# Performance work log

Measured on AMD Instinct MI355X. Metric: run time of the kernel, lower is better.

The kernel has to match this reference:

```python
import math
import jax, jax.numpy as jnp
import numpy as np

B, T, D = 512, 512, 256
ALPHA = 0.5
BETA = 0.9


def setup_inputs() -> dict:
    key = jax.random.key(0)
    ks = jax.random.split(key, 9)
    s = 1.0 / math.sqrt(D)
    return {
        "window_features": jax.random.normal(ks[0], (B, T, D), jnp.float32),
        "timestamps": jax.random.uniform(ks[1], (B, T), jnp.float32) * 86400.0 * 7,
        "prev_L": jax.random.normal(ks[2], (B, D), jnp.float32),
        "prev_M": jax.random.uniform(ks[3], (B, 1), jnp.float32),
        "pad_mask": jnp.zeros((B, T), jnp.bool_),
        "W_Q": jax.random.normal(ks[4], (D, D), jnp.float32) * s,
        "W_K": jax.random.normal(ks[5], (D, D), jnp.float32) * s,
        "W_V": jax.random.normal(ks[6], (D, D), jnp.float32) * s,
        "cls_w": jax.random.normal(ks[7], (1, 2 * D + 1), jnp.float32) * s,
        "cls_b": jnp.zeros((1,), jnp.float32),
    }


def reference(window_features, timestamps, prev_L, prev_M, pad_mask,
              W_Q, W_K, W_V, cls_w, cls_b):
    Bv, Tv, d = window_features.shape
    valid = ~pad_mask
    valid_f = valid.astype(window_features.dtype)              # [B,T]
    valid_count = jnp.clip(valid_f.sum(1, keepdims=True), 1.0)  # [B,1]

    # decay weights from recency (days)
    t_masked = jnp.where(pad_mask, -1e18, timestamps)
    t_max = t_masked.max(1, keepdims=True)                      # [B,1]
    dt = jnp.clip(t_max - timestamps, 0.0) / 86400.0
    lam = jnp.exp(-ALPHA * dt) * valid_f                        # [B,T]

    # mean-pooled query
    q = (window_features * valid_f[..., None]).sum(1) / valid_count  # [B,d]
    Q = q @ W_Q.T                                               # [B,d]
    K = jnp.einsum('btd,ed->bte', window_features, W_K)         # [B,T,d]
    V = jnp.einsum('btd,ed->bte', window_features, W_V)         # [B,T,d]

    scores = jnp.einsum('bd,btd->bt', Q, K) / math.sqrt(d)      # [B,T]
    scores = jnp.where(pad_mask, -1e9, scores)
    attn = jax.nn.softmax(scores, axis=-1)

    # decay-modulated reweighting + renormalization
    w = lam * attn
    w = w / (w.sum(1, keepdims=True) + 1e-8)

    L_t = jnp.einsum('bt,btd->bd', w, V)                        # [B,d]
    delta_t = L_t - prev_L
    M_t = BETA * prev_M + (1.0 - BETA) * jnp.linalg.norm(delta_t, axis=1, keepdims=True)
    T_event = jnp.concatenate([L_t, delta_t, M_t], axis=-1)     # [B,2d+1]
    p = (T_event @ cls_w.T + cls_b).squeeze(-1)                 # [B]
    return (p, T_event, L_t, M_t)
```

## Files before the change

kernel.cpp:

```cpp
#include <hip/hip_runtime.h>
#include <math.h>

#define ALPHA 0.5f
#define BETA 0.9f
#define Bsz 512
#define Tsz 512
#define Dsz 256
#define TILE 32
#define NTILE (Tsz / TILE)

__device__ __forceinline__ float wave_reduce_sum(float v) {
    v += __shfl_xor(v, 32, 64);
    v += __shfl_xor(v, 16, 64);
    v += __shfl_xor(v, 8, 64);
    v += __shfl_xor(v, 4, 64);
    v += __shfl_xor(v, 2, 64);
    v += __shfl_xor(v, 1, 64);
    return v;
}

__device__ __forceinline__ float wave_reduce_max(float v) {
    v = fmaxf(v, __shfl_xor(v, 32, 64));
    v = fmaxf(v, __shfl_xor(v, 16, 64));
    v = fmaxf(v, __shfl_xor(v, 8, 64));
    v = fmaxf(v, __shfl_xor(v, 4, 64));
    v = fmaxf(v, __shfl_xor(v, 2, 64));
    v = fmaxf(v, __shfl_xor(v, 1, 64));
    return v;
}

__device__ __forceinline__ void load_lds16(const float* g, float* l) {
    __builtin_amdgcn_global_load_lds(
        (const __attribute__((address_space(1))) void*)(g),
        (__attribute__((address_space(3))) void*)(l),
        16, 0, 0);
}

__global__ __launch_bounds__(256) void fused(const float* __restrict__ x,
                                             const float* __restrict__ ts,
                                             const unsigned char* __restrict__ pad,
                                             const float* __restrict__ WQ,
                                             const float* __restrict__ WK,
                                             const float* __restrict__ WV,
                                             const float* __restrict__ prevL,
                                             const float* __restrict__ prevM,
                                             const float* __restrict__ clsw,
                                             const float* __restrict__ clsb,
                                             float* __restrict__ out) {
    const int b = blockIdx.x;
    const int tid = threadIdx.x;
    const int w = tid >> 6, lane = tid & 63;
    const int rloc = lane >> 3;
    const int sub = lane & 7;

    __shared__ __align__(16) float buf[2][TILE][Dsz];
    __shared__ float lamS[Tsz];
    __shared__ float okS[Tsz];
    __shared__ float part[4][Dsz];
    __shared__ float qS[Dsz];
    __shared__ float QS[Dsz];
    __shared__ __align__(16) float qkS[Dsz];
    __shared__ float gS[TILE];
    __shared__ float xwS[Dsz];
    __shared__ float EGS[8];
    __shared__ float red[8];
    __shared__ float red2[4];
    __shared__ float tmaxS, cntS;

    float lmax = -1e30f;
    float lcnt = 0.f;
    for (int t = tid; t < Tsz; t += 256) {
        bool v = (pad[(size_t)b * Tsz + t] == 0);
        float tv = ts[(size_t)b * Tsz + t];
        okS[t] = v ? 1.f : 0.f;
        lamS[t] = tv;
        if (v) { lmax = fmaxf(lmax, tv); lcnt += 1.f; }
    }
    lmax = wave_reduce_max(lmax);
    lcnt = wave_reduce_sum(lcnt);
    if (lane == 0) { red[w] = lmax; red[4 + w] = lcnt; }
    __syncthreads();
    if (tid == 0) {
        tmaxS = fmaxf(fmaxf(red[0], red[1]), fmaxf(red[2], red[3]));
        cntS = fmaxf(red[4] + red[5] + red[6] + red[7], 1.f);
    }
    __syncthreads();

    const float tmax = tmaxS;
    for (int t = tid; t < Tsz; t += 256) {
        float dt = fmaxf(tmax - lamS[t], 0.f) * (1.f / 86400.f);
        lamS[t] = okS[t] * __expf(-ALPHA * dt);
    }

    const float* xb = x + (size_t)b * Tsz * Dsz;
    float4 a0 = make_float4(0.f, 0.f, 0.f, 0.f);
    float4 a1 = a0, a2 = a0, a3 = a0;
    const int tbase = w * 128;
    for (int i = 0; i < 128; i += 4) {
        const int t = tbase + i;
        float4 x0 = *(const float4*)(xb + (size_t)(t + 0) * Dsz + lane * 4);
        float4 x1 = *(const float4*)(xb + (size_t)(t + 1) * Dsz + lane * 4);
        float4 x2 = *(const float4*)(xb + (size_t)(t + 2) * Dsz + lane * 4);
        float4 x3 = *(const float4*)(xb + (size_t)(t + 3) * Dsz + lane * 4);
        const float v0 = okS[t], v1 = okS[t + 1], v2 = okS[t + 2], v3 = okS[t + 3];
        a0.x += v0 * x0.x; a0.y += v0 * x0.y; a0.z += v0 * x0.z; a0.w += v0 * x0.w;
        a1.x += v1 * x1.x; a1.y += v1 * x1.y; a1.z += v1 * x1.z; a1.w += v1 * x1.w;
        a2.x += v2 * x2.x; a2.y += v2 * x2.y; a2.z += v2 * x2.z; a2.w += v2 * x2.w;
        a3.x += v3 * x3.x; a3.y += v3 * x3.y; a3.z += v3 * x3.z; a3.w += v3 * x3.w;
    }
    float4 accq;
    accq.x = (a0.x + a1.x) + (a2.x + a3.x);
    accq.y = (a0.y + a1.y) + (a2.y + a3.y);
    accq.z = (a0.z + a1.z) + (a2.z + a3.z);
    accq.w = (a0.w + a1.w) + (a2.w + a3.w);
    part[w][lane * 4 + 0] = accq.x;
    part[w][lane * 4 + 1] = accq.y;
    part[w][lane * 4 + 2] = accq.z;
    part[w][lane * 4 + 3] = accq.w;

    {
        const int t0 = (NTILE - 1) * TILE;
        #pragma unroll
        for (int k = 0; k < 8; ++k) {
            const int r = w * 8 + k;
            load_lds16(xb + (size_t)(t0 + r) * Dsz + lane * 4, &buf[0][r][0]);
        }
    }
    __syncthreads();

    qS[tid] = (part[0][tid] + part[1][tid] + part[2][tid] + part[3][tid]) / cntS;
    __syncthreads();

    float Qi = 0.f;
    const float* wqrow = WQ + (size_t)tid * Dsz;
    #pragma unroll 4
    for (int d4 = 0; d4 < Dsz; d4 += 4) {
        float4 wv = *(const float4*)(wqrow + d4);
        Qi += wv.x * qS[d4] + wv.y * qS[d4 + 1] + wv.z * qS[d4 + 2] + wv.w * qS[d4 + 3];
    }
    QS[tid] = Qi;
    __syncthreads();

    {
        float v0 = 0.f, v1 = 0.f, v2 = 0.f, v3 = 0.f;
        #pragma unroll 4
        for (int e = 0; e < Dsz; e += 4) {
            v0 += QS[e + 0] * WK[(size_t)(e + 0) * Dsz + tid];
            v1 += QS[e + 1] * WK[(size_t)(e + 1) * Dsz + tid];
            v2 += QS[e + 2] * WK[(size_t)(e + 2) * Dsz + tid];
            v3 += QS[e + 3] * WK[(size_t)(e + 3) * Dsz + tid];
        }
        qkS[tid] = ((v0 + v1) + (v2 + v3)) * 0.0625f;
    }
    __syncthreads();

    float4 qkr[8];
    #pragma unroll
    for (int jj = 0; jj < 8; ++jj)
        qkr[jj] = *(const float4*)(&qkS[(jj * 8 + sub) << 2]);

    float4 acc = make_float4(0.f, 0.f, 0.f, 0.f);
    float E = 0.f, G = 0.f;
    int cur = 0;

    for (int it = 0; it < NTILE; ++it) {
        const int tile = (NTILE - 1) - it;

        if (it + 1 < NTILE) {
            const int t0 = (tile - 1) * TILE;
            #pragma unroll
            for (int k = 0; k < 8; ++k) {
                const int r = w * 8 + k;
                load_lds16(xb + (size_t)(t0 + r) * Dsz + lane * 4, &buf[cur ^ 1][r][0]);
            }
        }

        const int r = w * 8 + rloc;
        const float* rowp = &buf[cur][r][0];
        float s = 0.f;
        #pragma unroll
        for (int jj = 0; jj < 8; ++jj) {
            const float4 xv = *(const float4*)(rowp + ((jj * 8 + sub) << 2));
            s += xv.x * qkr[jj].x + xv.y * qkr[jj].y + xv.z * qkr[jj].z + xv.w * qkr[jj].w;
        }
        s += __shfl_xor(s, 1, 64);
        s += __shfl_xor(s, 2, 64);
        s += __shfl_xor(s, 4, 64);
        const int tglob = tile * TILE + r;
        const float e = okS[tglob] * __expf(s);
        const float g = lamS[tglob] * e;
        E += e; G += g;
        if (sub == 0) gS[r] = g;

        #pragma unroll
        for (int k = 0; k < 8; ++k) {
            const float g_k = gS[w * 8 + k];
            const float4 xv = *(const float4*)(&buf[cur][w * 8 + k][lane * 4]);
            acc.x += g_k * xv.x; acc.y += g_k * xv.y; acc.z += g_k * xv.z; acc.w += g_k * xv.w;
        }

        __syncthreads();
        cur ^= 1;
    }

    part[w][lane * 4 + 0] = acc.x;
    part[w][lane * 4 + 1] = acc.y;
    part[w][lane * 4 + 2] = acc.z;
    part[w][lane * 4 + 3] = acc.w;
    float Ew = wave_reduce_sum(E) * 0.125f;
    float Gw = wave_reduce_sum(G) * 0.125f;
    if (lane == 0) { EGS[w] = Ew; EGS[4 + w] = Gw; }
    __syncthreads();

    {
        float Et = EGS[0] + EGS[1] + EGS[2] + EGS[3];
        float Gt = EGS[4] + EGS[5] + EGS[6] + EGS[7];
        float denom = Gt + 1e-8f * Et;
        float accd = part[0][tid] + part[1][tid] + part[2][tid] + part[3][tid];
        xwS[tid] = (denom > 0.f) ? accd / denom : 0.f;
    }
    __syncthreads();

    float Le = 0.f;
    const float* wvrow = WV + (size_t)tid * Dsz;
    #pragma unroll 4
    for (int d4 = 0; d4 < Dsz; d4 += 4) {
        float4 wv = *(const float4*)(wvrow + d4);
        Le += wv.x * xwS[d4] + wv.y * xwS[d4 + 1] + wv.z * xwS[d4 + 2] + wv.w * xwS[d4 + 3];
    }
    float delta = Le - prevL[(size_t)b * Dsz + tid];

    float ssq = wave_reduce_sum(delta * delta);
    if (lane == 0) red[w] = ssq;
    __syncthreads();
    float nrm = sqrtf(red[0] + red[1] + red[2] + red[3]);
    float M = BETA * prevM[b] + (1.f - BETA) * nrm;

    float pp = Le * clsw[tid] + delta * clsw[Dsz + tid];
    float psum = wave_reduce_sum(pp);
    if (lane == 0) red2[w] = psum;
    __syncthreads();

    float* out_p = out;
    float* out_T = out + Bsz;
    float* out_L = out + Bsz + (size_t)Bsz * (2 * Dsz + 1);
    float* out_M = out + Bsz + (size_t)Bsz * (2 * Dsz + 1) + (size_t)Bsz * Dsz;

    out_T[(size_t)b * (2 * Dsz + 1) + tid] = Le;
    out_T[(size_t)b * (2 * Dsz + 1) + Dsz + tid] = delta;
    out_L[(size_t)b * Dsz + tid] = Le;
    if (tid == 0) {
        float p = red2[0] + red2[1] + red2[2] + red2[3] + M * clsw[2 * Dsz] + clsb[0];
        out_p[b] = p;
        out_T[(size_t)b * (2 * Dsz + 1) + 2 * Dsz] = M;
        out_M[b] = M;
    }
}

extern "C" void kernel_launch(void* const* d_in, const int* in_sizes, int n_in,
                              void* d_out, int out_size, void* d_ws, size_t ws_size,
                              hipStream_t stream) {
    const float* x     = (const float*)d_in[0];
    const float* ts    = (const float*)d_in[1];
    const float* prevL = (const float*)d_in[2];
    const float* prevM = (const float*)d_in[3];
    const unsigned char* pad = (const unsigned char*)d_in[4];
    const float* WQ    = (const float*)d_in[5];
    const float* WK    = (const float*)d_in[6];
    const float* WV    = (const float*)d_in[7];
    const float* clsw  = (const float*)d_in[8];
    const float* clsb  = (const float*)d_in[9];

    (void)d_ws; (void)ws_size;

    fused<<<Bsz, 256, 0, stream>>>(x, ts, pad, WQ, WK, WV, prevL, prevM, clsw, clsb,
                                   (float*)d_out);
}
```

Before: 442.2 us.

## Double block to 512 threads and drop LDS tile pipeline for direct loads

Launches 512 threads per batch row instead of 256 and splits each of the matvecs (WQ, WK, WV) across two halves with an LDS reduction. It also removes the 64KB double-buffered LDS tile and its per-tile barriers, so each wave streams its own 64 rows straight from global memory and broadcasts the row weights with shuffles. The aim is more waves in flight per CU to hide memory latency and no block-wide sync in the main loop. In exchange the x rows are read twice from global memory (once for scores, once for the weighted sum), which relies on cache hits.

```diff
diff --git a/kernel.cpp b/kernel.cpp
--- a/kernel.cpp
+++ b/kernel.cpp
@@ -6,8 +6,6 @@
 #define Bsz 512
 #define Tsz 512
 #define Dsz 256
-#define TILE 32
-#define NTILE (Tsz / TILE)
 
 __device__ __forceinline__ float wave_reduce_sum(float v) {
     v += __shfl_xor(v, 32, 64);
@@ -29,129 +27,122 @@
     return v;
 }
 
-__device__ __forceinline__ void load_lds16(const float* g, float* l) {
-    __builtin_amdgcn_global_load_lds(
-        (const __attribute__((address_space(1))) void*)(g),
-        (__attribute__((address_space(3))) void*)(l),
-        16, 0, 0);
-}
-
-__global__ __launch_bounds__(256) void fused(const float* __restrict__ x,
-                                             const float* __restrict__ ts,
-                                             const unsigned char* __restrict__ pad,
-                                             const float* __restrict__ WQ,
-                                             const float* __restrict__ WK,
-                                             const float* __restrict__ WV,
-                                             const float* __restrict__ prevL,
-                                             const float* __restrict__ prevM,
-                                             const float* __restrict__ clsw,
-                                             const float* __restrict__ clsb,
-                                             float* __restrict__ out) {
+__global__ __launch_bounds__(512, 4) void fused(const float* __restrict__ x,
+                                                const float* __restrict__ ts,
+                                                const unsigned char* __restrict__ pad,
+                                                const float* __restrict__ WQ,
+                                                const float* __restrict__ WK,
+                                                const float* __restrict__ WV,
+                                                const float* __restrict__ prevL,
+                                                const float* __restrict__ prevM,
+                                                const float* __restrict__ clsw,
+                                                const float* __restrict__ clsb,
+                                                float* __restrict__ out) {
     const int b = blockIdx.x;
     const int tid = threadIdx.x;
     const int w = tid >> 6, lane = tid & 63;
     const int rloc = lane >> 3;
     const int sub = lane & 7;
 
-    __shared__ __align__(16) float buf[2][TILE][Dsz];
     __shared__ float lamS[Tsz];
     __shared__ float okS[Tsz];
-    __shared__ float part[4][Dsz];
+    __shared__ float part[8][Dsz];
     __shared__ float qS[Dsz];
     __shared__ float QS[Dsz];
     __shared__ __align__(16) float qkS[Dsz];
-    __shared__ float gS[TILE];
     __shared__ float xwS[Dsz];
-    __shared__ float EGS[8];
-    __shared__ float red[8];
-    __shared__ float red2[4];
+    __shared__ float EGS[16];
+    __shared__ float red[16];
+    __shared__ float red2[8];
     __shared__ float tmaxS, cntS;
 
-    float lmax = -1e30f;
-    float lcnt = 0.f;
-    for (int t = tid; t < Tsz; t += 256) {
-        bool v = (pad[(size_t)b * Tsz + t] == 0);
-        float tv = ts[(size_t)b * Tsz + t];
-        okS[t] = v ? 1.f : 0.f;
-        lamS[t] = tv;
-        if (v) { lmax = fmaxf(lmax, tv); lcnt += 1.f; }
-    }
-    lmax = wave_reduce_max(lmax);
-    lcnt = wave_reduce_sum(lcnt);
-    if (lane == 0) { red[w] = lmax; red[4 + w] = lcnt; }
+    {
+        bool v = (pad[(size_t)b * Tsz + tid] == 0);
+        float tv = ts[(size_t)b * Tsz + tid];
+        okS[tid] = v ? 1.f : 0.f;
+        lamS[tid] = tv;
+        float lmax = v ? tv : -1e30f;
+        float lcnt = v ? 1.f : 0.f;
+        lmax = wave_reduce_max(lmax);
+        lcnt = wave_reduce_sum(lcnt);
+        if (lane == 0) { red[w] = lmax; red[8 + w] = lcnt; }
+    }
     __syncthreads();
     if (tid == 0) {
-        tmaxS = fmaxf(fmaxf(red[0], red[1]), fmaxf(red[2], red[3]));
-        cntS = fmaxf(red[4] + red[5] + red[6] + red[7], 1.f);
-    }
-    __syncthreads();
-
-    const float tmax = tmaxS;
-    for (int t = tid; t < Tsz; t += 256) {
-        float dt = fmaxf(tmax - lamS[t], 0.f) * (1.f / 86400.f);
-        lamS[t] = okS[t] * __expf(-ALPHA * dt);
+        float m = -1e30f, c = 0.f;
+        #pragma unroll
+        for (int i = 0; i < 8; ++i) { m = fmaxf(m, red[i]); c += red[8 + i]; }
+        tmaxS = m;
+        cntS = fmaxf(c, 1.f);
+    }
+    __syncthreads();
+    {
+        float dt = fmaxf(tmaxS - lamS[tid], 0.f) * (1.f / 86400.f);
+        lamS[tid] = okS[tid] * __expf(-ALPHA * dt);
     }
 
     const float* xb = x + (size_t)b * Tsz * Dsz;
-    float4 a0 = make_float4(0.f, 0.f, 0.f, 0.f);
-    float4 a1 = a0, a2 = a0, a3 = a0;
-    const int tbase = w * 128;
-    for (int i = 0; i < 128; i += 4) {
-        const int t = tbase + i;
-        float4 x0 = *(const float4*)(xb + (size_t)(t + 0) * Dsz + lane * 4);
-        float4 x1 = *(const float4*)(xb + (size_t)(t + 1) * Dsz + lane * 4);
-        float4 x2 = *(const float4*)(xb + (size_t)(t + 2) * Dsz + lane * 4);
-        float4 x3 = *(const float4*)(xb + (size_t)(t + 3) * Dsz + lane * 4);
-        const float v0 = okS[t], v1 = okS[t + 1], v2 = okS[t + 2], v3 = okS[t + 3];
-        a0.x += v0 * x0.x; a0.y += v0 * x0.y; a0.z += v0 * x0.z; a0.w += v0 * x0.w;
-        a1.x += v1 * x1.x; a1.y += v1 * x1.y; a1.z += v1 * x1.z; a1.w += v1 * x1.w;
-        a2.x += v2 * x2.x; a2.y += v2 * x2.y; a2.z += v2 * x2.z; a2.w += v2 * x2.w;
-        a3.x += v3 * x3.x; a3.y += v3 * x3.y; a3.z += v3 * x3.z; a3.w += v3 * x3.w;
-    }
-    float4 accq;
-    accq.x = (a0.x + a1.x) + (a2.x + a3.x);
-    accq.y = (a0.y + a1.y) + (a2.y + a3.y);
-    accq.z = (a0.z + a1.z) + (a2.z + a3.z);
-    accq.w = (a0.w + a1.w) + (a2.w + a3.w);
-    part[w][lane * 4 + 0] = accq.x;
-    part[w][lane * 4 + 1] = accq.y;
-    part[w][lane * 4 + 2] = accq.z;
-    part[w][lane * 4 + 3] = accq.w;
-
-    {
-        const int t0 = (NTILE - 1) * TILE;
-        #pragma unroll
-        for (int k = 0; k < 8; ++k) {
-            const int r = w * 8 + k;
-            load_lds16(xb + (size_t)(t0 + r) * Dsz + lane * 4, &buf[0][r][0]);
-        }
-    }
-    __syncthreads();
-
-    qS[tid] = (part[0][tid] + part[1][tid] + part[2][tid] + part[3][tid]) / cntS;
-    __syncthreads();
-
-    float Qi = 0.f;
-    const float* wqrow = WQ + (size_t)tid * Dsz;
-    #pragma unroll 4
-    for (int d4 = 0; d4 < Dsz; d4 += 4) {
-        float4 wv = *(const float4*)(wqrow + d4);
-        Qi += wv.x * qS[d4] + wv.y * qS[d4 + 1] + wv.z * qS[d4 + 2] + wv.w * qS[d4 + 3];
-    }
-    QS[tid] = Qi;
-    __syncthreads();
-
-    {
+    {
+        float4 a0 = make_float4(0.f, 0.f, 0.f, 0.f);
+        float4 a1 = a0, a2 = a0, a3 = a0;
+        const int tbase = w * 64;
+        for (int i = 0; i < 64; i += 4) {
+            const int t = tbase + i;
+            float4 x0 = *(const float4*)(xb + (size_t)(t + 0) * Dsz + lane * 4);
+            float4 x1 = *(const float4*)(xb + (size_t)(t + 1) * Dsz + lane * 4);
+            float4 x2 = *(const float4*)(xb + (size_t)(t + 2) * Dsz + lane * 4);
+            float4 x3 = *(const float4*)(xb + (size_t)(t + 3) * Dsz + lane * 4);
+            const float v0 = okS[t], v1 = okS[t + 1], v2 = okS[t + 2], v3 = okS[t + 3];
+            a0.x += v0 * x0.x; a0.y += v0 * x0.y; a0.z += v0 * x0.z; a0.w += v0 * x0.w;
+            a1.x += v1 * x1.x; a1.y += v1 * x1.y; a1.z += v1 * x1.z; a1.w += v1 * x1.w;
+            a2.x += v2 * x2.x; a2.y += v2 * x2.y; a2.z += v2 * x2.z; a2.w += v2 * x2.w;
+            a3.x += v3 * x3.x; a3.y += v3 * x3.y; a3.z += v3 * x3.z; a3.w += v3 * x3.w;
+        }
+        part[w][lane * 4 + 0] = (a0.x + a1.x) + (a2.x + a3.x);
+        part[w][lane * 4 + 1] = (a0.y + a1.y) + (a2.y + a3.y);
+        part[w][lane * 4 + 2] = (a0.z + a1.z) + (a2.z + a3.z);
+        part[w][lane * 4 + 3] = (a0.w + a1.w) + (a2.w + a3.w);
+    }
+    __syncthreads();
+    if (tid < Dsz) {
+        float s = 0.f;
+        #pragma unroll
+        for (int w2 = 0; w2 < 8; ++w2) s += part[w2][tid];
+        qS[tid] = s / cntS;
+    }
+    __syncthreads();
+
+    {
+        const int i = tid & 255, half = tid >> 8;
+        const float* wq = WQ + (size_t)i * Dsz + half * 128;
+        const float* qh = qS + half * 128;
+        float acc = 0.f;
+        #pragma unroll 4
+        for (int d4 = 0; d4 < 128; d4 += 4) {
+            float4 wv = *(const float4*)(wq + d4);
+            acc += wv.x * qh[d4] + wv.y * qh[d4 + 1] + wv.z * qh[d4 + 2] + wv.w * qh[d4 + 3];
+        }
+        part[half][i] = acc;
+    }
+    __syncthreads();
+    if (tid < Dsz) QS[tid] = part[0][tid] + part[1][tid];
+    __syncthreads();
+
+    {
+        const int d = tid & 255, half = tid >> 8;
+        const int e0 = half * 128;
         float v0 = 0.f, v1 = 0.f, v2 = 0.f, v3 = 0.f;
         #pragma unroll 4
-        for (int e = 0; e < Dsz; e += 4) {
-            v0 += QS[e + 0] * WK[(size_t)(e + 0) * Dsz + tid];
-            v1 += QS[e + 1] * WK[(size_t)(e + 1) * Dsz + tid];
-            v2 += QS[e + 2] * WK[(size_t)(e + 2) * Dsz + tid];
-            v3 += QS[e + 3] * WK[(size_t)(e + 3) * Dsz + tid];
-        }
-        qkS[tid] = ((v0 + v1) + (v2 + v3)) * 0.0625f;
-    }
+        for (int e = e0; e < e0 + 128; e += 4) {
+            v0 += QS[e + 0] * WK[(size_t)(e + 0) * Dsz + d];
+            v1 += QS[e + 1] * WK[(size_t)(e + 1) * Dsz + d];
+            v2 += QS[e + 2] * WK[(size_t)(e + 2) * Dsz + d];
+            v3 += QS[e + 3] * WK[(size_t)(e + 3) * Dsz + d];
+        }
+        part[half][d] = (v0 + v1) + (v2 + v3);
+    }
+    __syncthreads();
+    if (tid < Dsz) qkS[tid] = (part[0][tid] + part[1][tid]) * 0.0625f;
     __syncthreads();
 
     float4 qkr[8];
@@ -161,99 +152,103 @@
 
     float4 acc = make_float4(0.f, 0.f, 0.f, 0.f);
     float E = 0.f, G = 0.f;
-    int cur = 0;
-
-    for (int it = 0; it < NTILE; ++it) {
-        const int tile = (NTILE - 1) - it;
-
-        if (it + 1 < NTILE) {
-            const int t0 = (tile - 1) * TILE;
+    {
+        const int rowbase = w * 64;
+        for (int gi = 7; gi >= 0; --gi) {
+            const int base = rowbase + gi * 8;
+            const int r = base + rloc;
+            const float* rp = xb + (size_t)r * Dsz;
+            float s = 0.f;
+            #pragma unroll
+            for (int jj = 0; jj < 8; ++jj) {
+                const float4 xv = *(const float4*)(rp + ((jj * 8 + sub) << 2));
+                s += xv.x * qkr[jj].x + xv.y * qkr[jj].y + xv.z * qkr[jj].z + xv.w * qkr[jj].w;
+            }
+            s += __shfl_xor(s, 1, 64);
+            s += __shfl_xor(s, 2, 64);
+            s += __shfl_xor(s, 4, 64);
+            const float e = okS[r] * __expf(s);
+            const float g = lamS[r] * e;
+            E += e; G += g;
             #pragma unroll
             for (int k = 0; k < 8; ++k) {
-                const int r = w * 8 + k;
-                load_lds16(xb + (size_t)(t0 + r) * Dsz + lane * 4, &buf[cur ^ 1][r][0]);
+                const float gk = __shfl(g, k * 8, 64);
+                const float4 xa = *(const float4*)(xb + (size_t)(base + k) * Dsz + lane * 4);
+                acc.x += gk * xa.x; acc.y += gk * xa.y; acc.z += gk * xa.z; acc.w += gk * xa.w;
             }
         }
-
-        const int r = w * 8 + rloc;
-        const float* rowp = &buf[cur][r][0];
-        float s = 0.f;
-        #pragma unroll
-        for (int jj = 0; jj < 8; ++jj) {
-            const float4 xv = *(const float4*)(rowp + ((jj * 8 + sub) << 2));
-            s += xv.x * qkr[jj].x + xv.y * qkr[jj].y + xv.z * qkr[jj].z + xv.w * qkr[jj].w;
-        }
-        s += __shfl_xor(s, 1, 64);
-        s += __shfl_xor(s, 2, 64);
-        s += __shfl_xor(s, 4, 64);
-        const int tglob = tile * TILE + r;
-        const float e = okS[tglob] * __expf(s);
-        const float g = lamS[tglob] * e;
-        E += e; G += g;
-        if (sub == 0) gS[r] = g;
-
-        #pragma unroll
-        for (int k = 0; k < 8; ++k) {
-            const float g_k = gS[w * 8 + k];
-            const float4 xv = *(const float4*)(&buf[cur][w * 8 + k][lane * 4]);
-            acc.x += g_k * xv.x; acc.y += g_k * xv.y; acc.z += g_k * xv.z; acc.w += g_k * xv.w;
-        }
-
-        __syncthreads();
-        cur ^= 1;
-    }
-
+    }
     part[w][lane * 4 + 0] = acc.x;
     part[w][lane * 4 + 1] = acc.y;
     part[w][lane * 4 + 2] = acc.z;
     part[w][lane * 4 + 3] = acc.w;
-    float Ew = wave_reduce_sum(E) * 0.125f;
-    float Gw = wave_reduce_sum(G) * 0.125f;
-    if (lane == 0) { EGS[w] = Ew; EGS[4 + w] = Gw; }
-    __syncthreads();
-
-    {
-        float Et = EGS[0] + EGS[1] + EGS[2] + EGS[3];
-        float Gt = EGS[4] + EGS[5] + EGS[6] + EGS[7];
+    {
+        float Ew = wave_reduce_sum(E) * 0.125f;
+        float Gw = wave_reduce_sum(G) * 0.125f;
+        if (lane == 0) { EGS[w] = Ew; EGS[8 + w] = Gw; }
+    }
+    __syncthreads();
+    if (tid < Dsz) {
+        float Et = 0.f, Gt = 0.f;
+        #pragma unroll
+        for (int i = 0; i < 8; ++i) { Et += EGS[i]; Gt += EGS[8 + i]; }
         float denom = Gt + 1e-8f * Et;
-        float accd = part[0][tid] + part[1][tid] + part[2][tid] + part[3][tid];
+        float accd = 0.f;
+        #pragma unroll
+        for (int w2 = 0; w2 < 8; ++w2) accd += part[w2][tid];
         xwS[tid] = (denom > 0.f) ? accd / denom : 0.f;
     }
     __syncthreads();
 
-    float Le = 0.f;
-    const float* wvrow = WV + (size_t)tid * Dsz;
-    #pragma unroll 4
-    for (int d4 = 0; d4 < Dsz; d4 += 4) {
-        float4 wv = *(const float4*)(wvrow + d4);
-        Le += wv.x * xwS[d4] + wv.y * xwS[d4 + 1] + wv.z * xwS[d4 + 2] + wv.w * xwS[d4 + 3];
-    }
-    float delta = Le - prevL[(size_t)b * Dsz + tid];
-
+    {
+        const int i = tid & 255, half = tid >> 8;
+        const float* wv = WV + (size_t)i * Dsz + half * 128;
+        const float* xh = xwS + half * 128;
+        float a = 0.f;
+        #pragma unroll 4
+        for (int d4 = 0; d4 < 128; d4 += 4) {
+            float4 wvv = *(const float4*)(wv + d4);
+            a += wvv.x * xh[d4] + wvv.y * xh[d4 + 1] + wvv.z * xh[d4 + 2] + wvv.w * xh[d4 + 3];
+        }
+        part[half][i] = a;
+    }
+    __syncthreads();
+
+    float Le = 0.f, delta = 0.f, pp = 0.f;
+    if (tid < Dsz) {
+        Le = part[0][tid] + part[1][tid];
+        delta = Le - prevL[(size_t)b * Dsz + tid];
+        pp = Le * clsw[tid] + delta * clsw[Dsz + tid];
+    }
     float ssq = wave_reduce_sum(delta * delta);
-    if (lane == 0) red[w] = ssq;
-    __syncthreads();
-    float nrm = sqrtf(red[0] + red[1] + red[2] + red[3]);
-    float M = BETA * prevM[b] + (1.f - BETA) * nrm;
-
-    float pp = Le * clsw[tid] + delta * clsw[Dsz + tid];
     float psum = wave_reduce_sum(pp);
-    if (lane == 0) red2[w] = psum;
-    __syncthreads();
-
-    float* out_p = out;
-    float* out_T = out + Bsz;
-    float* out_L = out + Bsz + (size_t)Bsz * (2 * Dsz + 1);
-    float* out_M = out + Bsz + (size_t)Bsz * (2 * Dsz + 1) + (size_t)Bsz * Dsz;
-
-    out_T[(size_t)b * (2 * Dsz + 1) + tid] = Le;
-    out_T[(size_t)b * (2 * Dsz + 1) + Dsz + tid] = delta;
-    out_L[(size_t)b * Dsz + tid] = Le;
-    if (tid == 0) {
-        float p = red2[0] + red2[1] + red2[2] + red2[3] + M * clsw[2 * Dsz] + clsb[0];
-        out_p[b] = p;
-        out_T[(size_t)b * (2 * Dsz + 1) + 2 * Dsz] = M;
-        out_M[b] = M;
+    if (lane == 0) { red[w] = ssq; red2[w] = psum; }
+    __syncthreads();
+
+    if (tid < Dsz) {
+        float sr = 0.f;
+        #pragma unroll
+        for (int i = 0; i < 8; ++i) sr += red[i];
+        float nrm = sqrtf(sr);
+        float M = BETA * prevM[b] + (1.f - BETA) * nrm;
+
+        float* out_p = out;
+        float* out_T = out + Bsz;
+        float* out_L = out + Bsz + (size_t)Bsz * (2 * Dsz + 1);
+        float* out_M = out + Bsz + (size_t)Bsz * (2 * Dsz + 1) + (size_t)Bsz * Dsz;
+
+        out_T[(size_t)b * (2 * Dsz + 1) + tid] = Le;
+        out_T[(size_t)b * (2 * Dsz + 1) + Dsz + tid] = delta;
+        out_L[(size_t)b * Dsz + tid] = Le;
+        if (tid == 0) {
+            float ps = 0.f;
+            #pragma unroll
+            for (int i = 0; i < 8; ++i) ps += red2[i];
+            float p = ps + M * clsw[2 * Dsz] + clsb[0];
+            out_p[b] = p;
+            out_T[(size_t)b * (2 * Dsz + 1) + 2 * Dsz] = M;
+            out_M[b] = M;
+        }
     }
 }
 
@@ -273,6 +268,6 @@
 
     (void)d_ws; (void)ws_size;
 
-    fused<<<Bsz, 256, 0, stream>>>(x, ts, pad, WQ, WK, WV, prevL, prevM, clsw, clsb,
+    fused<<<Bsz, 512, 0, stream>>>(x, ts, pad, WQ, WK, WV, prevL, prevM, clsw, clsb,
                                    (float*)d_out);
 }
```

New measurement: 464.0 us. 4.9% more time.
